# Optimization experiments

Measured on AMD Instinct MI355X. Metric: run time of the kernel, lower is better.

Reference implementation:

```python
import jax, jax.numpy as jnp
import numpy as np

N_NODES = 32768
N_EDGES = 262144
HEAD = 8
CHANNEL = 64
LAYER_NUM = 2
HC = HEAD * CHANNEL  # 512


def setup_inputs() -> dict:
    key = jax.random.key(0)
    ks = jax.random.split(key, 12)
    def lin(k, fan_in, fan_out):
        s = 1.0 / np.sqrt(fan_in)
        kw, kb = jax.random.split(k)
        W = jax.random.uniform(kw, (fan_in, fan_out), jnp.float32, -s, s)
        b = jax.random.uniform(kb, (fan_out,), jnp.float32, -s, s)
        return W, b
    Wn, bn = lin(ks[0], 118, HC)
    We, be = lin(ks[1], 22, HC)
    Wa, ba = lin(ks[2], 2 * HC, HC)
    attn_w = jax.random.normal(ks[3], (1, HEAD, CHANNEL), jnp.float32) * 0.1
    x = jax.random.normal(ks[4], (N_NODES, 118), jnp.float32)
    edge_feat = jax.random.normal(ks[5], (N_EDGES, 22), jnp.float32)
    src = jax.random.randint(ks[6], (N_EDGES,), 0, N_NODES)
    dst = jax.random.randint(ks[7], (N_EDGES,), 0, N_NODES)
    return {"x": x, "edge_feat": edge_feat, "src": src, "dst": dst,
            "Wn": Wn, "bn": bn, "We": We, "be": be, "Wa": Wa, "ba": ba,
            "attn_w": attn_w}


def reference(x, edge_feat, src, dst, Wn, bn, We, be, Wa, ba, attn_w):
    N = x.shape[0]
    H, C = attn_w.shape[1], attn_w.shape[2]
    h = x @ Wn + bn                      # [N, H*C]
    _eh = edge_feat @ We + be            # computed in original forward, never used
    for _ in range(LAYER_NUM):
        # gather src/dst node states onto edges and score them (GATv2 style)
        e = jnp.concatenate([h[src], h[dst]], axis=-1)            # [E, 2HC]
        e = jax.nn.leaky_relu(e @ Wa + ba, negative_slope=0.01)   # [E, HC]
        score = jnp.sum(e.reshape(-1, H, C) * attn_w, axis=-1)    # [E, H]
        # edge softmax normalized over incoming edges of each dst node
        m = jax.ops.segment_max(score, dst, num_segments=N)       # [N, H]
        ex = jnp.exp(score - m[dst])                              # [E, H]
        denom = jax.ops.segment_sum(ex, dst, num_segments=N)      # [N, H]
        alpha = ex / denom[dst]                                   # [E, H]
        # weighted message passing: u_mul_e then sum over dst
        msg = h[src].reshape(-1, H, C) * alpha[:, :, None]        # [E, H, C]
        h = jax.ops.segment_sum(msg, dst, num_segments=N).reshape(N, H * C)
    return h
```

## Files before the change

### kernel.cpp

```cpp
#include <hip/hip_runtime.h>
#include <hip/hip_bf16.h>
#include <stdint.h>

#define N_NODES 32768
#define N_EDGES 262144

typedef __attribute__((ext_vector_type(8))) short short8;
typedef __attribute__((ext_vector_type(4))) float f32x4;
typedef __attribute__((ext_vector_type(4))) uint u32x4;

typedef const __attribute__((address_space(1))) void* gvp;
typedef __attribute__((address_space(3))) void* lvp;

#define LDH 1536

__device__ __forceinline__ float bf2f(ushort u) {
  return __uint_as_float(((uint)u) << 16);
}
__device__ __forceinline__ ushort f2bf(float f) {
  uint x = __float_as_uint(f);
  uint r = (x + 0x7fffu + ((x >> 16) & 1u)) >> 16;
  return (ushort)r;
}
__device__ __forceinline__ float loadf(const void* p, size_t i, int isbf) {
  return isbf ? bf2f(((const ushort*)p)[i]) : ((const float*)p)[i];
}

__global__ void detect_dtype(const uint* __restrict__ xw, int* __restrict__ flag) {
  __shared__ int cnt;
  if (threadIdx.x == 0) cnt = 0;
  __syncthreads();
  int good = 0;
  for (int i = threadIdx.x; i < 1024; i += 256) {
    uint lo = xw[i] & 0xFFFFu;
    uint ef = (lo >> 7) & 0xFFu;
    if (lo == 0u || (ef >= 0x60u && ef <= 0x90u)) good++;
  }
  atomicAdd(&cnt, good);
  __syncthreads();
  if (threadIdx.x == 0) *flag = (cnt >= 614) ? 1 : 0;
}

__global__ void prep_all(const void* __restrict__ Wa, const void* __restrict__ Wn,
                         const void* __restrict__ ba, const void* __restrict__ bn,
                         const void* __restrict__ aw, const void* __restrict__ x,
                         const int* __restrict__ flag, const int* __restrict__ dst,
                         ushort* __restrict__ W2T, ushort* __restrict__ BTc,
                         ushort* __restrict__ Wn_pad, float* __restrict__ bias2,
                         float* __restrict__ bnf, float* __restrict__ wf,
                         float* __restrict__ zbias, ushort* __restrict__ xp,
                         int* __restrict__ cnt) {
  const int b = blockIdx.x;
  if (b >= 2564 + 16384) {
    int e = (b - 2564 - 16384) * 256 + threadIdx.x;
    atomicAdd(&cnt[dst[e]], 1);
    return;
  }
  const int fl = *flag;
  if (b < 2048) {
    int t = b * 256 + threadIdx.x;
    int n = t >> 9, k = t & 511;
    size_t idx = (n < 512) ? ((size_t)k * 512 + n) : ((size_t)(512 + k) * 512 + (n - 512));
    W2T[t] = f2bf(loadf(Wa, idx, fl));
  } else if (b < 2304) {
    int t = (b - 2048) * 256 + threadIdx.x;
    int n = t >> 7, k = t & 127;
    BTc[t] = (k < 118) ? f2bf(loadf(Wn, (size_t)k * 512 + n, fl)) : (ushort)0;
  } else if (b < 2560) {
    int t = (b - 2304) * 256 + threadIdx.x;
    int n = t >> 9, j = t & 511;
    Wn_pad[t] = (n < 118) ? f2bf(loadf(Wn, (size_t)n * 512 + j, fl)) : (ushort)0;
  } else if (b < 2564) {
    int t = (b - 2560) * 256 + threadIdx.x;
    if (t < 1024) bias2[t] = (t < 512) ? loadf(ba, t, fl) : 0.f;
    if (t < 512) { bnf[t] = loadf(bn, t, fl); wf[t] = loadf(aw, t, fl); }
    if (t < 128) zbias[t] = 0.f;
  } else {
    int t = (b - 2564) * 256 + threadIdx.x;
    int i = t >> 7, k = t & 127;
    xp[t] = (k < 118) ? f2bf(loadf(x, (size_t)i * 118 + k, fl)) : (ushort)0;
  }
}

__global__ __launch_bounds__(256)
void build_bc(const ushort* __restrict__ W2T, const float* __restrict__ bnf,
              const float* __restrict__ bias2, float* __restrict__ bcomb) {
  const int tid = blockIdx.x * 256 + threadIdx.x;
  if (tid < 512) bcomb[tid] = bnf[tid];
  const int wave = threadIdx.x >> 6, lane = threadIdx.x & 63;
  const int j = blockIdx.x * 4 + wave;
  const uint4 v = *(const uint4*)(W2T + (size_t)j * 512 + lane * 8);
  const float4 b0 = *(const float4*)(bnf + lane * 8);
  const float4 b1 = *(const float4*)(bnf + lane * 8 + 4);
  const uint w[4] = {v.x, v.y, v.z, v.w};
  const float bb[8] = {b0.x, b0.y, b0.z, b0.w, b1.x, b1.y, b1.z, b1.w};
  float s = 0.f;
#pragma unroll
  for (int i = 0; i < 4; ++i) {
    s += __uint_as_float(w[i] << 16) * bb[2 * i];
    s += __uint_as_float(w[i] & 0xffff0000u) * bb[2 * i + 1];
  }
  s += __shfl_xor(s, 1);  s += __shfl_xor(s, 2);  s += __shfl_xor(s, 4);
  s += __shfl_xor(s, 8);  s += __shfl_xor(s, 16); s += __shfl_xor(s, 32);
  if (lane == 0) bcomb[512 + j] = s + bias2[j];
}

__global__ __launch_bounds__(1024)
void csr_scan(const int* __restrict__ cnt, int* __restrict__ rowptr,
              int* __restrict__ cursor) {
  __shared__ int part[1024];
  const int t = threadIdx.x;
  const int base = t * 32;
  int loc[32];
  int s = 0;
#pragma unroll
  for (int i = 0; i < 32; ++i) { loc[i] = s; s += cnt[base + i]; }
  part[t] = s;
  __syncthreads();
  for (int off = 1; off < 1024; off <<= 1) {
    int v = (t >= off) ? part[t - off] : 0;
    __syncthreads();
    part[t] += v;
    __syncthreads();
  }
  int pre = (t == 0) ? 0 : part[t - 1];
#pragma unroll
  for (int i = 0; i < 32; ++i) {
    int v = pre + loc[i];
    rowptr[base + i] = v;
    cursor[base + i] = v;
  }
  if (t == 1023) rowptr[N_NODES] = part[1023];
}

__global__ void csr_fill(const int* __restrict__ dst, const int* __restrict__ src,
                         int* __restrict__ cursor, int* __restrict__ esrc) {
  int e = blockIdx.x * blockDim.x + threadIdx.x;
  int p = atomicAdd(&cursor[dst[e]], 1);
  esrc[p] = src[e];
}

__global__ __launch_bounds__(256)
void gemm_bf16(const ushort* __restrict__ A, const ushort* __restrict__ BT,
               const float* __restrict__ bias, ushort* __restrict__ C,
               int M, int N, int K, int lda, int ldc) {
  __shared__ __align__(16) ushort As[128 * 32];
  __shared__ __align__(16) ushort Bs[128 * 32];
  const int tid = threadIdx.x, wave = tid >> 6, lane = tid & 63;
  const int bm = blockIdx.y * 128, bn = blockIdx.x * 128;
  const int wm = (wave >> 1) * 64, wn = (wave & 1) * 64;
  const int fcol = lane & 15, quad = lane >> 4;

  const f32x4 zero = {0.f, 0.f, 0.f, 0.f};
  f32x4 acc[4][4];
#pragma unroll
  for (int i = 0; i < 4; ++i)
#pragma unroll
    for (int j = 0; j < 4; ++j) acc[i][j] = zero;

  for (int k0 = 0; k0 < K; k0 += 32) {
#pragma unroll
    for (int r = 0; r < 2; ++r) {
      int o = r * 4096 + wave * 1024 + lane * 16;
      int row = o >> 6;
      int ke = (o & 63) >> 1;
      const ushort* gA = A + (size_t)(bm + row) * lda + k0 + ke;
      const ushort* gB = BT + (size_t)(bn + row) * K + k0 + ke;
      ushort* lA = As + ((r * 4096 + wave * 1024) >> 1);
      ushort* lB = Bs + ((r * 4096 + wave * 1024) >> 1);
      __builtin_amdgcn_global_load_lds((gvp)(const void*)gA, (lvp)(void*)lA, 16, 0, 0);
      __builtin_amdgcn_global_load_lds((gvp)(const void*)gB, (lvp)(void*)lB, 16, 0, 0);
    }
    __syncthreads();
    short8 a[4], b[4];
#pragma unroll
    for (int i = 0; i < 4; ++i) {
      a[i] = *(const short8*)&As[(wm + i * 16 + fcol) * 32 + quad * 8];
      b[i] = *(const short8*)&Bs[(wn + i * 16 + fcol) * 32 + quad * 8];
    }
#pragma unroll
    for (int i = 0; i < 4; ++i)
#pragma unroll
      for (int j = 0; j < 4; ++j)
        acc[i][j] = __builtin_amdgcn_mfma_f32_16x16x32_bf16(a[i], b[j], acc[i][j], 0, 0, 0);
    __syncthreads();
  }

#pragma unroll
  for (int i = 0; i < 4; ++i) {
    int rowb = bm + wm + i * 16 + quad * 4;
#pragma unroll
    for (int j = 0; j < 4; ++j) {
      int col = bn + wn + j * 16 + fcol;
      float bb = bias[col];
#pragma unroll
      for (int r = 0; r < 4; ++r) {
        C[(size_t)(rowb + r) * ldc + col] = f2bf(acc[i][j][r] + bb);
      }
    }
  }
}

__global__ __launch_bounds__(256)
void node_fused_l1(const ushort* __restrict__ HP, const int* __restrict__ esrc,
                   const int* __restrict__ rowptr, const float* __restrict__ wf,
                   const float* __restrict__ bias2, ushort* __restrict__ HP2) {
  const int wave = threadIdx.x >> 6, lane = threadIdx.x & 63;
  const int d = blockIdx.x * 4 + wave;
  const int beg = rowptr[d], end = rowptr[d + 1];
  const int c0 = lane * 8;

  const uint4 qv = *(const uint4*)(HP + (size_t)d * LDH + 1024 + c0);
  const uint qw[4] = {qv.x, qv.y, qv.z, qv.w};
  float q[8], w[8];
#pragma unroll
  for (int i = 0; i < 4; ++i) {
    q[2 * i]     = __uint_as_float(qw[i] << 16);
    q[2 * i + 1] = __uint_as_float(qw[i] & 0xffff0000u);
  }
  const float4 w0 = *(const float4*)(wf + c0);
  const float4 w1 = *(const float4*)(wf + c0 + 4);
  w[0] = w0.x; w[1] = w0.y; w[2] = w0.z; w[3] = w0.w;
  w[4] = w1.x; w[5] = w1.y; w[6] = w1.z; w[7] = w1.w;

  float m = -3e38f, den = 0.f;
  float aP[8], aQ[8], aH[8];
#pragma unroll
  for (int i = 0; i < 8; ++i) { aP[i] = 0.f; aQ[i] = 0.f; aH[i] = 0.f; }

  if (beg < end) {
    int sj = esrc[beg];
    for (int j = beg; j < end; ++j) {
      const int s = sj;
      if (j + 1 < end) sj = esrc[j + 1];
      const ushort* row = HP + (size_t)s * LDH;
      const uint4 hv = *(const uint4*)(row + c0);
      const uint4 pa = *(const uint4*)(row + 512 + c0);
      const uint4 pb = *(const uint4*)(row + 1024 + c0);
      const uint paw[4] = {pa.x, pa.y, pa.z, pa.w};
      const uint pbw[4] = {pb.x, pb.y, pb.z, pb.w};
      const uint hw[4]  = {hv.x, hv.y, hv.z, hv.w};
      float t = 0.f;
#pragma unroll
      for (int i = 0; i < 4; ++i) {
        float ea = __uint_as_float(paw[i] << 16) + q[2 * i];
        float eb = __uint_as_float(paw[i] & 0xffff0000u) + q[2 * i + 1];
        ea = (ea > 0.f) ? ea : 0.01f * ea;
        eb = (eb > 0.f) ? eb : 0.01f * eb;
        t += ea * w[2 * i] + eb * w[2 * i + 1];
      }
      t += __shfl_xor(t, 1);
      t += __shfl_xor(t, 2);
      t += __shfl_xor(t, 4);
      if (__any(t > m)) {
        const float mnew = fmaxf(m, t);
        const float corr = __expf(m - mnew);
        const float ex = __expf(t - mnew);
        den = den * corr + ex;
#pragma unroll
        for (int i = 0; i < 4; ++i) {
          aP[2 * i]     = aP[2 * i] * corr     + ex * __uint_as_float(paw[i] << 16);
          aP[2 * i + 1] = aP[2 * i + 1] * corr + ex * __uint_as_float(paw[i] & 0xffff0000u);
          aQ[2 * i]     = aQ[2 * i] * corr     + ex * __uint_as_float(pbw[i] << 16);
          aQ[2 * i + 1] = aQ[2 * i + 1] * corr + ex * __uint_as_float(pbw[i] & 0xffff0000u);
          aH[2 * i]     = aH[2 * i] * corr     + ex * __uint_as_float(hw[i] << 16);
          aH[2 * i + 1] = aH[2 * i + 1] * corr + ex * __uint_as_float(hw[i] & 0xffff0000u);
        }
        m = mnew;
      } else {
        const float ex = __expf(t - m);
        den += ex;
#pragma unroll
        for (int i = 0; i < 4; ++i) {
          aP[2 * i]     += ex * __uint_as_float(paw[i] << 16);
          aP[2 * i + 1] += ex * __uint_as_float(paw[i] & 0xffff0000u);
          aQ[2 * i]     += ex * __uint_as_float(pbw[i] << 16);
          aQ[2 * i + 1] += ex * __uint_as_float(pbw[i] & 0xffff0000u);
          aH[2 * i]     += ex * __uint_as_float(hw[i] << 16);
          aH[2 * i + 1] += ex * __uint_as_float(hw[i] & 0xffff0000u);
        }
      }
    }
  }

  const int deg = end - beg;
  const float inv = deg ? (1.f / den) : 0.f;
  const float4 bp0 = *(const float4*)(bias2 + c0);
  const float4 bp1 = *(const float4*)(bias2 + c0 + 4);
  const float bp[8] = {bp0.x, bp0.y, bp0.z, bp0.w, bp1.x, bp1.y, bp1.z, bp1.w};
  uint oP[4], oQ[4], oH[4];
#pragma unroll
  for (int i = 0; i < 4; ++i) {
    float p0 = deg ? aP[2 * i] * inv : bp[2 * i];
    float p1 = deg ? aP[2 * i + 1] * inv : bp[2 * i + 1];
    float q0 = deg ? aQ[2 * i] * inv : 0.f;
    float q1 = deg ? aQ[2 * i + 1] * inv : 0.f;
    float h0v = aH[2 * i] * inv, h1v = aH[2 * i + 1] * inv;
    oP[i] = (uint)f2bf(p0) | ((uint)f2bf(p1) << 16);
    oQ[i] = (uint)f2bf(q0) | ((uint)f2bf(q1) << 16);
    oH[i] = (uint)f2bf(h0v) | ((uint)f2bf(h1v) << 16);
  }
  u32x4 vP = {oP[0], oP[1], oP[2], oP[3]};
  u32x4 vQ = {oQ[0], oQ[1], oQ[2], oQ[3]};
  u32x4 vH = {oH[0], oH[1], oH[2], oH[3]};
  ushort* orow = HP2 + (size_t)d * LDH;
  *(u32x4*)(orow + c0) = vH;
  *(u32x4*)(orow + 512 + c0) = vP;
  *(u32x4*)(orow + 1024 + c0) = vQ;
}

__global__ __launch_bounds__(256)
void node_fused_l2(const ushort* __restrict__ HP2, const int* __restrict__ esrc,
                   const int* __restrict__ rowptr, const float* __restrict__ wf,
                   const int* __restrict__ flag, void* __restrict__ out) {
  const int wave = threadIdx.x >> 6, lane = threadIdx.x & 63;
  const int d = blockIdx.x * 4 + wave;
  const int beg = rowptr[d], end = rowptr[d + 1];
  const int c0 = lane * 8;

  const uint4 qv = *(const uint4*)(HP2 + (size_t)d * LDH + 1024 + c0);
  const uint qw[4] = {qv.x, qv.y, qv.z, qv.w};
  float q[8], w[8];
#pragma unroll
  for (int i = 0; i < 4; ++i) {
    q[2 * i]     = __uint_as_float(qw[i] << 16);
    q[2 * i + 1] = __uint_as_float(qw[i] & 0xffff0000u);
  }
  const float4 w0 = *(const float4*)(wf + c0);
  const float4 w1 = *(const float4*)(wf + c0 + 4);
  w[0] = w0.x; w[1] = w0.y; w[2] = w0.z; w[3] = w0.w;
  w[4] = w1.x; w[5] = w1.y; w[6] = w1.z; w[7] = w1.w;

  float m = -3e38f, den = 0.f;
  float acc[8] = {0.f, 0.f, 0.f, 0.f, 0.f, 0.f, 0.f, 0.f};

  if (beg < end) {
    int sj = esrc[beg];
    for (int j = beg; j < end; ++j) {
      const int s = sj;
      if (j + 1 < end) sj = esrc[j + 1];
      const ushort* row = HP2 + (size_t)s * LDH;
      const uint4 hv = *(const uint4*)(row + c0);
      const uint4 pv = *(const uint4*)(row + 512 + c0);
      const uint pw[4] = {pv.x, pv.y, pv.z, pv.w};
      const uint hw[4] = {hv.x, hv.y, hv.z, hv.w};
      float t = 0.f;
#pragma unroll
      for (int i = 0; i < 4; ++i) {
        float ea = __uint_as_float(pw[i] << 16) + q[2 * i];
        float eb = __uint_as_float(pw[i] & 0xffff0000u) + q[2 * i + 1];
        ea = (ea > 0.f) ? ea : 0.01f * ea;
        eb = (eb > 0.f) ? eb : 0.01f * eb;
        t += ea * w[2 * i] + eb * w[2 * i + 1];
      }
      t += __shfl_xor(t, 1);
      t += __shfl_xor(t, 2);
      t += __shfl_xor(t, 4);
      if (__any(t > m)) {
        const float mnew = fmaxf(m, t);
        const float corr = __expf(m - mnew);
        const float ex = __expf(t - mnew);
        den = den * corr + ex;
#pragma unroll
        for (int i = 0; i < 4; ++i) {
          acc[2 * i]     = acc[2 * i] * corr     + ex * __uint_as_float(hw[i] << 16);
          acc[2 * i + 1] = acc[2 * i + 1] * corr + ex * __uint_as_float(hw[i] & 0xffff0000u);
        }
        m = mnew;
      } else {
        const float ex = __expf(t - m);
        den += ex;
#pragma unroll
        for (int i = 0; i < 4; ++i) {
          acc[2 * i]     += ex * __uint_as_float(hw[i] << 16);
          acc[2 * i + 1] += ex * __uint_as_float(hw[i] & 0xffff0000u);
        }
      }
    }
  }

  const float inv = (end > beg) ? (1.f / den) : 0.f;
  if (*flag) {
    uint o[4];
#pragma unroll
    for (int i = 0; i < 4; ++i) {
      float v0 = acc[2 * i] * inv, v1 = acc[2 * i + 1] * inv;
      o[i] = (uint)f2bf(v0) | ((uint)f2bf(v1) << 16);
    }
    u32x4 ov = {o[0], o[1], o[2], o[3]};
    __builtin_nontemporal_store(ov, (u32x4*)((ushort*)out + (size_t)d * 512 + c0));
  } else {
    f32x4 f0 = {acc[0] * inv, acc[1] * inv, acc[2] * inv, acc[3] * inv};
    f32x4 f1 = {acc[4] * inv, acc[5] * inv, acc[6] * inv, acc[7] * inv};
    __builtin_nontemporal_store(f0, (f32x4*)((float*)out + (size_t)d * 512 + c0));
    __builtin_nontemporal_store(f1, (f32x4*)((float*)out + (size_t)d * 512 + c0 + 4));
  }
}

extern "C" void kernel_launch(void* const* d_in, const int* in_sizes, int n_in,
                              void* d_out, int out_size, void* d_ws, size_t ws_size,
                              hipStream_t stream) {
  const void* x   = d_in[0];
  const int*  src = (const int*)d_in[2];
  const int*  dst = (const int*)d_in[3];
  const void* Wn  = d_in[4];
  const void* bn  = d_in[5];
  const void* Wa  = d_in[8];
  const void* ba  = d_in[9];
  const void* aw  = d_in[10];

  char* ws = (char*)d_ws;
  size_t off = 0;
  auto alloc = [&](size_t bytes) {
    char* p = ws + off;
    off = (off + bytes + 255) & ~(size_t)255;
    return p;
  };
  ushort* HP     = (ushort*)alloc((size_t)N_NODES * LDH * 2);
  ushort* HP2    = (ushort*)alloc((size_t)N_NODES * LDH * 2);
  int*    esrc   = (int*)   alloc((size_t)N_EDGES * 4);
  int*    rowptr = (int*)   alloc((size_t)(N_NODES + 1) * 4);
  int*    cnt    = (int*)   alloc((size_t)N_NODES * 4);
  int*    cursor = (int*)   alloc((size_t)N_NODES * 4);
  ushort* W2T    = (ushort*)alloc((size_t)1024 * 512 * 2);
  ushort* BTc    = (ushort*)alloc((size_t)1536 * 128 * 2);
  ushort* Wn_pad = (ushort*)alloc((size_t)128 * 512 * 2);
  float*  bias2  = (float*) alloc(1024 * 4);
  float*  bcomb  = (float*) alloc(1536 * 4);
  float*  zbias  = (float*) alloc(128 * 4);
  ushort* xp     = (ushort*)alloc((size_t)N_NODES * 128 * 2);
  float*  bnf    = (float*) alloc(512 * 4);
  float*  wf     = (float*) alloc(512 * 4);
  int*    flag   = (int*)   alloc(256);

  detect_dtype<<<1, 256, 0, stream>>>((const uint*)x, flag);
  hipMemsetAsync(cnt, 0, (size_t)N_NODES * 4, stream);
  prep_all<<<2564 + 16384 + 1024, 256, 0, stream>>>(
      Wa, Wn, ba, bn, aw, x, flag, dst, W2T, BTc, Wn_pad, bias2, bnf, wf, zbias,
      xp, cnt);
  build_bc<<<256, 256, 0, stream>>>(W2T, bnf, bias2, bcomb);
  {
    dim3 g(128 / 128, 1024 / 128);
    gemm_bf16<<<g, 256, 0, stream>>>(W2T, Wn_pad, zbias, BTc + 512 * 128,
                                     1024, 128, 512, 512, 128);
  }
  csr_scan<<<1, 1024, 0, stream>>>(cnt, rowptr, cursor);
  csr_fill<<<N_EDGES / 256, 256, 0, stream>>>(dst, src, cursor, esrc);

  {
    dim3 g(1536 / 128, N_NODES / 128);
    gemm_bf16<<<g, 256, 0, stream>>>(xp, BTc, bcomb, HP,
                                     N_NODES, 1536, 128, 128, LDH);
  }

  node_fused_l1<<<N_NODES / 4, 256, 0, stream>>>(HP, esrc, rowptr, wf, bias2, HP2);
  node_fused_l2<<<N_NODES / 4, 256, 0, stream>>>(HP2, esrc, rowptr, wf, flag, d_out);
}
```

Measured before the change: 426.8 us.

## Merge prep kernels into fewer launches and split layer-2 Q into separate array

Folds the cnt memset into the dtype-detection kernel. It also merges build_bc, the small weight GEMM and the CSR scan into one mid kernel, and merges csr_fill with the main node GEMM into one launch, cutting the pipeline from about 9 launches to 6. Layer-2 node state drops from a 1536-wide stride to a 1024-wide H/P array plus a separate Q array, so the per-edge gathers touch a denser buffer. The scan now runs as one 256-thread block, which lengthens the serial per-thread loop; the merged kernels also mix heterogeneous block roles.

```diff
diff --git a/kernel.cpp b/kernel.cpp
--- a/kernel.cpp
+++ b/kernel.cpp
@@ -13,6 +13,7 @@
 typedef __attribute__((address_space(3))) void* lvp;
 
 #define LDH 1536
+#define LDH2 1024
 
 __device__ __forceinline__ float bf2f(ushort u) {
   return __uint_as_float(((uint)u) << 16);
@@ -26,9 +27,15 @@
   return isbf ? bf2f(((const ushort*)p)[i]) : ((const float*)p)[i];
 }
 
-__global__ void detect_dtype(const uint* __restrict__ xw, int* __restrict__ flag) {
-  __shared__ int cnt;
-  if (threadIdx.x == 0) cnt = 0;
+__global__ void detect_init(const uint* __restrict__ xw, int* __restrict__ flag,
+                            int* __restrict__ cnt) {
+  if (blockIdx.x > 0) {
+    int i = (blockIdx.x - 1) * 256 + threadIdx.x;
+    if (i < N_NODES) cnt[i] = 0;
+    return;
+  }
+  __shared__ int c;
+  if (threadIdx.x == 0) c = 0;
   __syncthreads();
   int good = 0;
   for (int i = threadIdx.x; i < 1024; i += 256) {
@@ -36,9 +43,9 @@
     uint ef = (lo >> 7) & 0xFFu;
     if (lo == 0u || (ef >= 0x60u && ef <= 0x90u)) good++;
   }
-  atomicAdd(&cnt, good);
+  atomicAdd(&c, good);
   __syncthreads();
-  if (threadIdx.x == 0) *flag = (cnt >= 614) ? 1 : 0;
+  if (threadIdx.x == 0) *flag = (c >= 614) ? 1 : 0;
 }
 
 __global__ void prep_all(const void* __restrict__ Wa, const void* __restrict__ Wn,
@@ -82,72 +89,14 @@
   }
 }
 
-__global__ __launch_bounds__(256)
-void build_bc(const ushort* __restrict__ W2T, const float* __restrict__ bnf,
-              const float* __restrict__ bias2, float* __restrict__ bcomb) {
-  const int tid = blockIdx.x * 256 + threadIdx.x;
-  if (tid < 512) bcomb[tid] = bnf[tid];
-  const int wave = threadIdx.x >> 6, lane = threadIdx.x & 63;
-  const int j = blockIdx.x * 4 + wave;
-  const uint4 v = *(const uint4*)(W2T + (size_t)j * 512 + lane * 8);
-  const float4 b0 = *(const float4*)(bnf + lane * 8);
-  const float4 b1 = *(const float4*)(bnf + lane * 8 + 4);
-  const uint w[4] = {v.x, v.y, v.z, v.w};
-  const float bb[8] = {b0.x, b0.y, b0.z, b0.w, b1.x, b1.y, b1.z, b1.w};
-  float s = 0.f;
-#pragma unroll
-  for (int i = 0; i < 4; ++i) {
-    s += __uint_as_float(w[i] << 16) * bb[2 * i];
-    s += __uint_as_float(w[i] & 0xffff0000u) * bb[2 * i + 1];
-  }
-  s += __shfl_xor(s, 1);  s += __shfl_xor(s, 2);  s += __shfl_xor(s, 4);
-  s += __shfl_xor(s, 8);  s += __shfl_xor(s, 16); s += __shfl_xor(s, 32);
-  if (lane == 0) bcomb[512 + j] = s + bias2[j];
-}
-
-__global__ __launch_bounds__(1024)
-void csr_scan(const int* __restrict__ cnt, int* __restrict__ rowptr,
-              int* __restrict__ cursor) {
-  __shared__ int part[1024];
-  const int t = threadIdx.x;
-  const int base = t * 32;
-  int loc[32];
-  int s = 0;
-#pragma unroll
-  for (int i = 0; i < 32; ++i) { loc[i] = s; s += cnt[base + i]; }
-  part[t] = s;
-  __syncthreads();
-  for (int off = 1; off < 1024; off <<= 1) {
-    int v = (t >= off) ? part[t - off] : 0;
-    __syncthreads();
-    part[t] += v;
-    __syncthreads();
-  }
-  int pre = (t == 0) ? 0 : part[t - 1];
-#pragma unroll
-  for (int i = 0; i < 32; ++i) {
-    int v = pre + loc[i];
-    rowptr[base + i] = v;
-    cursor[base + i] = v;
-  }
-  if (t == 1023) rowptr[N_NODES] = part[1023];
-}
-
-__global__ void csr_fill(const int* __restrict__ dst, const int* __restrict__ src,
-                         int* __restrict__ cursor, int* __restrict__ esrc) {
-  int e = blockIdx.x * blockDim.x + threadIdx.x;
-  int p = atomicAdd(&cursor[dst[e]], 1);
-  esrc[p] = src[e];
-}
-
-__global__ __launch_bounds__(256)
-void gemm_bf16(const ushort* __restrict__ A, const ushort* __restrict__ BT,
-               const float* __restrict__ bias, ushort* __restrict__ C,
-               int M, int N, int K, int lda, int ldc) {
+__device__ __forceinline__ void gemm_body(
+    const ushort* __restrict__ A, const ushort* __restrict__ BT,
+    const float* __restrict__ bias, ushort* __restrict__ C,
+    int M, int N, int K, int lda, int ldc, int bx, int by) {
   __shared__ __align__(16) ushort As[128 * 32];
   __shared__ __align__(16) ushort Bs[128 * 32];
   const int tid = threadIdx.x, wave = tid >> 6, lane = tid & 63;
-  const int bm = blockIdx.y * 128, bn = blockIdx.x * 128;
+  const int bm = by * 128, bn = bx * 128;
   const int wm = (wave >> 1) * 64, wn = (wave & 1) * 64;
   const int fcol = lane & 15, quad = lane >> 4;
 
@@ -202,9 +151,80 @@
 }
 
 __global__ __launch_bounds__(256)
+void mid_kernel(const ushort* __restrict__ W2T, const ushort* __restrict__ Wn_pad,
+                const float* __restrict__ bnf, const float* __restrict__ bias2,
+                const float* __restrict__ zbias, float* __restrict__ bcomb,
+                ushort* __restrict__ BTc, const int* __restrict__ cnt,
+                int* __restrict__ rowptr, int* __restrict__ cursor) {
+  const int b = blockIdx.x;
+  if (b < 256) {
+    const int tid = b * 256 + threadIdx.x;
+    if (tid < 512) bcomb[tid] = bnf[tid];
+    const int wave = threadIdx.x >> 6, lane = threadIdx.x & 63;
+    const int j = b * 4 + wave;
+    const uint4 v = *(const uint4*)(W2T + (size_t)j * 512 + lane * 8);
+    const float4 b0 = *(const float4*)(bnf + lane * 8);
+    const float4 b1 = *(const float4*)(bnf + lane * 8 + 4);
+    const uint w[4] = {v.x, v.y, v.z, v.w};
+    const float bb[8] = {b0.x, b0.y, b0.z, b0.w, b1.x, b1.y, b1.z, b1.w};
+    float s = 0.f;
+#pragma unroll
+    for (int i = 0; i < 4; ++i) {
+      s += __uint_as_float(w[i] << 16) * bb[2 * i];
+      s += __uint_as_float(w[i] & 0xffff0000u) * bb[2 * i + 1];
+    }
+    s += __shfl_xor(s, 1);  s += __shfl_xor(s, 2);  s += __shfl_xor(s, 4);
+    s += __shfl_xor(s, 8);  s += __shfl_xor(s, 16); s += __shfl_xor(s, 32);
+    if (lane == 0) bcomb[512 + j] = s + bias2[j];
+  } else if (b < 264) {
+    gemm_body(W2T, Wn_pad, zbias, BTc + 512 * 128, 1024, 128, 512, 512, 128,
+              0, b - 256);
+  } else {
+    __shared__ int part[256];
+    const int t = threadIdx.x;
+    const int base = t * 128;
+    int s = 0;
+    for (int i = 0; i < 128; ++i) s += cnt[base + i];
+    part[t] = s;
+    __syncthreads();
+    for (int off = 1; off < 256; off <<= 1) {
+      int v = (t >= off) ? part[t - off] : 0;
+      __syncthreads();
+      part[t] += v;
+      __syncthreads();
+    }
+    int run = (t == 0) ? 0 : part[t - 1];
+    for (int i = 0; i < 128; ++i) {
+      int v = cnt[base + i];
+      rowptr[base + i] = run;
+      cursor[base + i] = run;
+      run += v;
+    }
+    if (t == 255) rowptr[N_NODES] = part[255];
+  }
+}
+
+__global__ __launch_bounds__(256)
+void fill_gemm(const int* __restrict__ dst, const int* __restrict__ src,
+               int* __restrict__ cursor, int* __restrict__ esrc,
+               const ushort* __restrict__ xp, const ushort* __restrict__ BTc,
+               const float* __restrict__ bcomb, ushort* __restrict__ HP) {
+  const int b = blockIdx.x;
+  if (b < 1024) {
+    int e = b * 256 + threadIdx.x;
+    int p = atomicAdd(&cursor[dst[e]], 1);
+    esrc[p] = src[e];
+    return;
+  }
+  const int gi = b - 1024;
+  gemm_body(xp, BTc, bcomb, HP, N_NODES, 1536, 128, 128, LDH, gi % 12, gi / 12);
+}
+
+__global__ __launch_bounds__(256)
 void node_fused_l1(const ushort* __restrict__ HP, const int* __restrict__ esrc,
                    const int* __restrict__ rowptr, const float* __restrict__ wf,
-                   const float* __restrict__ bias2, ushort* __restrict__ HP2) {
+                   const float* __restrict__ bias2, ushort* __restrict__ HP2,
+                   ushort* __restrict__ Q2arr) {
   const int wave = threadIdx.x >> 6, lane = threadIdx.x & 63;
   const int d = blockIdx.x * 4 + wave;
   const int beg = rowptr[d], end = rowptr[d + 1];
@@ -303,22 +323,23 @@
   u32x4 vP = {oP[0], oP[1], oP[2], oP[3]};
   u32x4 vQ = {oQ[0], oQ[1], oQ[2], oQ[3]};
   u32x4 vH = {oH[0], oH[1], oH[2], oH[3]};
-  ushort* orow = HP2 + (size_t)d * LDH;
+  ushort* orow = HP2 + (size_t)d * LDH2;
   *(u32x4*)(orow + c0) = vH;
   *(u32x4*)(orow + 512 + c0) = vP;
-  *(u32x4*)(orow + 1024 + c0) = vQ;
+  *(u32x4*)(Q2arr + (size_t)d * 512 + c0) = vQ;
 }
 
 __global__ __launch_bounds__(256)
-void node_fused_l2(const ushort* __restrict__ HP2, const int* __restrict__ esrc,
-                   const int* __restrict__ rowptr, const float* __restrict__ wf,
-                   const int* __restrict__ flag, void* __restrict__ out) {
+void node_fused_l2(const ushort* __restrict__ HP2, const ushort* __restrict__ Q2arr,
+                   const int* __restrict__ esrc, const int* __restrict__ rowptr,
+                   const float* __restrict__ wf, const int* __restrict__ flag,
+                   void* __restrict__ out) {
   const int wave = threadIdx.x >> 6, lane = threadIdx.x & 63;
   const int d = blockIdx.x * 4 + wave;
   const int beg = rowptr[d], end = rowptr[d + 1];
   const int c0 = lane * 8;
 
-  const uint4 qv = *(const uint4*)(HP2 + (size_t)d * LDH + 1024 + c0);
+  const uint4 qv = *(const uint4*)(Q2arr + (size_t)d * 512 + c0);
   const uint qw[4] = {qv.x, qv.y, qv.z, qv.w};
   float q[8], w[8];
 #pragma unroll
@@ -339,7 +360,7 @@
     for (int j = beg; j < end; ++j) {
       const int s = sj;
       if (j + 1 < end) sj = esrc[j + 1];
-      const ushort* row = HP2 + (size_t)s * LDH;
+      const ushort* row = HP2 + (size_t)s * LDH2;
       const uint4 hv = *(const uint4*)(row + c0);
       const uint4 pv = *(const uint4*)(row + 512 + c0);
       const uint pw[4] = {pv.x, pv.y, pv.z, pv.w};
@@ -417,7 +438,8 @@
     return p;
   };
   ushort* HP     = (ushort*)alloc((size_t)N_NODES * LDH * 2);
-  ushort* HP2    = (ushort*)alloc((size_t)N_NODES * LDH * 2);
+  ushort* HP2    = (ushort*)alloc((size_t)N_NODES * LDH2 * 2);
+  ushort* Q2arr  = (ushort*)alloc((size_t)N_NODES * 512 * 2);
   int*    esrc   = (int*)   alloc((size_t)N_EDGES * 4);
   int*    rowptr = (int*)   alloc((size_t)(N_NODES + 1) * 4);
   int*    cnt    = (int*)   alloc((size_t)N_NODES * 4);
@@ -433,26 +455,16 @@
   float*  wf     = (float*) alloc(512 * 4);
   int*    flag   = (int*)   alloc(256);
 
-  detect_dtype<<<1, 256, 0, stream>>>((const uint*)x, flag);
-  hipMemsetAsync(cnt, 0, (size_t)N_NODES * 4, stream);
+  detect_init<<<1 + 128, 256, 0, stream>>>((const uint*)x, flag, cnt);
   prep_all<<<2564 + 16384 + 1024, 256, 0, stream>>>(
       Wa, Wn, ba, bn, aw, x, flag, dst, W2T, BTc, Wn_pad, bias2, bnf, wf, zbias,
       xp, cnt);
-  build_bc<<<256, 256, 0, stream>>>(W2T, bnf, bias2, bcomb);
-  {
-    dim3 g(128 / 128, 1024 / 128);
-    gemm_bf16<<<g, 256, 0, stream>>>(W2T, Wn_pad, zbias, BTc + 512 * 128,
-                                     1024, 128, 512, 512, 128);
-  }
-  csr_scan<<<1, 1024, 0, stream>>>(cnt, rowptr, cursor);
-  csr_fill<<<N_EDGES / 256, 256, 0, stream>>>(dst, src, cursor, esrc);
-
-  {
-    dim3 g(1536 / 128, N_NODES / 128);
-    gemm_bf16<<<g, 256, 0, stream>>>(xp, BTc, bcomb, HP,
-                                     N_NODES, 1536, 128, 128, LDH);
-  }
-
-  node_fused_l1<<<N_NODES / 4, 256, 0, stream>>>(HP, esrc, rowptr, wf, bias2, HP2);
-  node_fused_l2<<<N_NODES / 4, 256, 0, stream>>>(HP2, esrc, rowptr, wf, flag, d_out);
-}
+  mid_kernel<<<256 + 8 + 1, 256, 0, stream>>>(W2T, Wn_pad, bnf, bias2, zbias,
+                                              bcomb, BTc, cnt, rowptr, cursor);
+  fill_gemm<<<1024 + 12 * 256, 256, 0, stream>>>(dst, src, cursor, esrc, xp, BTc,
+                                                 bcomb, HP);
+  node_fused_l1<<<N_NODES / 4, 256, 0, stream>>>(HP, esrc, rowptr, wf, bias2,
+                                                 HP2, Q2arr);
+  node_fused_l2<<<N_NODES / 4, 256, 0, stream>>>(HP2, Q2arr, esrc, rowptr, wf,
+                                                 flag, d_out);
+}
```

Result: faster. 406.5 us (-4.7%).
